# Optimization experiments

Hardware: AMD Instinct MI355X
Metric: run time of the kernel (lower is better)

## Reference

```python
import jax, jax.numpy as jnp
import numpy as np

ORDER = 3  # cubic B-splines, matching BSpline(..., 3)


def bspline_basis(x, t, order):
    """Cox-de Boor recursion, vectorized over batch and features.

    x: [B, F] evaluation points
    t: [F, M] sorted knot vectors (M = num_basis + order + 1)
    returns: [B, F, M-1-order] basis values B_j^{order}(x), zero outside the
    base interval [t[order], t[M-1-order]] (scipy extrapolate=False + nan_to_num).
    """
    M = t.shape[-1]
    xd = x[:, :, None]            # [B, F, 1]
    tb = t[None, :, :]            # [1, F, M]
    # degree-0 indicator functions: [B, F, M-1]
    B = ((xd >= tb[:, :, :-1]) & (xd < tb[:, :, 1:])).astype(x.dtype)
    for d in range(1, order + 1):
        t0 = tb[:, :, : M - d - 1]   # t_j
        td = tb[:, :, d : M - 1]     # t_{j+d}
        t1 = tb[:, :, 1 : M - d]     # t_{j+1}
        td1 = tb[:, :, d + 1 : M]    # t_{j+d+1}
        den1 = td - t0
        den2 = td1 - t1
        w1 = jnp.where(den1 > 0, (xd - t0) / jnp.where(den1 > 0, den1, 1.0), 0.0)
        w2 = jnp.where(den2 > 0, (td1 - xd) / jnp.where(den2 > 0, den2, 1.0), 0.0)
        B = w1 * B[:, :, : M - d - 1] + w2 * B[:, :, 1 : M - d]
    # zero outside the base interval [t[order], t[n]] (scipy NaN -> nan_to_num -> 0)
    lo = t[None, :, order]           # [1, F]
    hi = t[None, :, M - 1 - order]   # [1, F]
    valid = ((x >= lo) & (x <= hi)).astype(x.dtype)  # [B, F]
    return B * valid[:, :, None]


def setup_inputs() -> dict:
    key = jax.random.key(0)
    k_x, k_w, k_b = jax.random.split(key, 3)
    batch, in_features, out_features, num_basis = 4096, 512, 512, 30
    x = jax.random.normal(k_x, (batch, in_features), dtype=jnp.float32)
    knots = jnp.broadcast_to(
        jnp.linspace(-2.0, 2.0, num_basis + ORDER + 1, dtype=jnp.float32),
        (in_features, num_basis + ORDER + 1),
    )
    weights = jax.random.normal(k_w, (out_features, in_features, num_basis), dtype=jnp.float32)
    bias = jax.random.normal(k_b, (out_features,), dtype=jnp.float32)
    return {"x": x, "knots": knots, "weights": weights, "bias": bias}


def reference(x, knots, weights, bias):
    ks = jnp.sort(knots, axis=-1)              # module sorts knots before eval
    basis = bspline_basis(x, ks, ORDER)        # [B, F, num_basis]
    out = jnp.einsum("bij,kij->bk", basis, weights)
    return out + bias
```

## Files before the change

### kernel.cpp

```cpp
#include <hip/hip_runtime.h>
#include <hip/hip_bf16.h>
#include <stdint.h>


#define BATCH 4096
#define INF   512
#define OUTF  512
#define NB    30
#define NBP   32
#define NKNOT 34
#define KDIMP (INF * NBP)

#define BM 128
#define BN 128
#define BK 64
#define KSPLIT 8
#define KCHUNK (KDIMP / KSPLIT)
#define NT     (KCHUNK / BK)
#define FPC    (KCHUNK / NBP)

typedef short v8s __attribute__((ext_vector_type(8)));
typedef float v4f __attribute__((ext_vector_type(4)));

__device__ __forceinline__ unsigned short f2bf(float f) {
  uint32_t u = __float_as_uint(f);
  uint32_t r = (u + 0x7fffu + ((u >> 16) & 1u)) >> 16;
  return (unsigned short)r;
}

__device__ __forceinline__ void gload16(const unsigned short* g, unsigned short* l) {
  auto gp = reinterpret_cast<const __attribute__((address_space(1))) unsigned short*>(
      reinterpret_cast<uintptr_t>(g));
  auto lp = reinterpret_cast<__attribute__((address_space(3))) unsigned short*>(
      reinterpret_cast<uintptr_t>(l));
  __builtin_amdgcn_global_load_lds(gp, lp, 16, 0, 0);
}

__global__ __launch_bounds__(256) void w_cast_kernel(const float* __restrict__ in,
                                                     unsigned short* __restrict__ out) {
  int idx = blockIdx.x * 256 + threadIdx.x;
  int k   = idx >> 13;
  int rem = idx & 8191;
  int i   = rem >> 4;
  int jp  = rem & 15;
  int j   = jp * 2;
  const float* src = in + ((size_t)k * INF + i) * NB;
  float lo = (j     < NB) ? src[j]     : 0.f;
  float hi = (j + 1 < NB) ? src[j + 1] : 0.f;
  ((uint32_t*)out)[idx] = (uint32_t)f2bf(lo) | ((uint32_t)f2bf(hi) << 16);
}

__global__ __launch_bounds__(256) void basis_kernel(const float* __restrict__ x,
                                                    const float* __restrict__ knots,
                                                    uint2* __restrict__ valsT,
                                                    unsigned char* __restrict__ j0T) {
  __shared__ float tile[32][33];
  int b0 = blockIdx.x * 32;
  int f0 = blockIdx.y * 32;
  int lx = threadIdx.x & 31;
  int ly = threadIdx.x >> 5;
  #pragma unroll
  for (int q = 0; q < 4; ++q)
    tile[ly + q * 8][lx] = x[(size_t)(b0 + ly + q * 8) * INF + f0 + lx];
  __syncthreads();
  #pragma unroll
  for (int q = 0; q < 4; ++q) {
    int fy = ly + q * 8;
    float xv = tile[lx][fy];
    const float* tk = knots + (size_t)(f0 + fy) * NKNOT;
    uint2 pv = {0u, 0u};
    int j0 = 0;
    float tlo = tk[3], thi = tk[30];
    if (xv >= tlo && xv <= thi) {
      float t0v = tk[0];
      float h   = tk[1] - t0v;
      int m = (int)floorf((xv - t0v) * __builtin_amdgcn_rcpf(h));
      m = m < 3 ? 3 : (m > 30 ? 30 : m);
      while (m > 3 && xv < tk[m]) --m;
      while (m < 30 && xv >= tk[m + 1]) ++m;
      float Nv[4], left[4], right[4];
      Nv[0] = 1.f;
      #pragma unroll
      for (int d = 1; d <= 3; ++d) {
        left[d]  = xv - tk[m + 1 - d];
        right[d] = tk[m + d] - xv;
        float saved = 0.f;
        #pragma unroll
        for (int r = 0; r < d; ++r) {
          float temp = Nv[r] * __builtin_amdgcn_rcpf(right[r + 1] + left[d - r]);
          Nv[r] = saved + right[r + 1] * temp;
          saved = left[d - r] * temp;
        }
        Nv[d] = saved;
      }
      j0 = m - 3;
      pv.x = (uint32_t)f2bf(Nv[0]) | ((uint32_t)f2bf(Nv[1]) << 16);
      pv.y = (uint32_t)f2bf(Nv[2]) | ((uint32_t)f2bf(Nv[3]) << 16);
    }
    size_t oi = (size_t)(f0 + fy) * BATCH + b0 + lx;
    valsT[oi] = pv;
    j0T[oi]   = (unsigned char)j0;
  }
}

__global__ __launch_bounds__(256) void bias_kernel(const float* __restrict__ bias,
                                                   float* __restrict__ out) {
  int idx = blockIdx.x * 256 + threadIdx.x;
  out[idx] = bias[idx & (OUTF - 1)];
}

__device__ __forceinline__ void writeA(unsigned short* Abuf, int eb, int hf,
                                       uint2 v, int j0) {
  unsigned rowb = (unsigned)eb * 128;
  unsigned x7   = (unsigned)(eb & 7);
  char* base = (char*)Abuf;
  uint4 z = {0u, 0u, 0u, 0u};
  #pragma unroll
  for (int s = 0; s < 4; ++s) {
    unsigned slot = ((unsigned)(hf * 4 + s)) ^ x7;
    *(uint4*)(base + rowb + (slot << 4)) = z;
  }
  int d0 = hf * 16 + (j0 >> 1);
  #define WR32(d, val) { unsigned by = (unsigned)(d) * 4u; \
    *(uint32_t*)(base + rowb + ((((by >> 4) ^ x7) << 4) | (by & 15u))) = (val); }
  if (j0 & 1) {
    WR32(d0,     v.x << 16);
    WR32(d0 + 1, (v.x >> 16) | (v.y << 16));
    WR32(d0 + 2, v.y >> 16);
  } else {
    WR32(d0,     v.x);
    WR32(d0 + 1, v.y);
  }
  #undef WR32
}

__global__ __launch_bounds__(256, 4) void gemm_kernel(const uint2* __restrict__ valsT,
                                                      const unsigned char* __restrict__ j0T,
                                                      const unsigned short* __restrict__ Bt,
                                                      float* __restrict__ C) {
  __shared__ unsigned short As[BM * BK];
  __shared__ unsigned short Bs[BN * BK];
  int tid  = threadIdx.x;
  int lane = tid & 63;
  int w    = tid >> 6;

  int bid = blockIdx.x;
  int swz = (bid & 7) * 128 + (bid >> 3);
  int bn  = swz >> 8;
  int rem = swz & 255;
  int ks  = rem >> 5;
  int bm  = rem & 31;

  int row0 = bm * BM;
  int col0 = bn * BN;
  int kk0  = ks * KCHUNK;
  int fbase = ks * FPC;

  int eb = tid & 127;
  int hf = tid >> 7;
  size_t vidx0 = (size_t)(fbase + hf) * BATCH + row0 + eb;

  int lrow = lane >> 3;
  int lseg = (lane & 7) ^ lrow;
  const unsigned short* gb = Bt + (size_t)(col0 + w * 8 + lrow) * KDIMP + kk0 + lseg * 8;
  unsigned short* lB = &Bs[w * 512];

  v4f acc[4][4];
  #pragma unroll
  for (int i = 0; i < 4; ++i)
    #pragma unroll
    for (int j = 0; j < 4; ++j)
      acc[i][j] = (v4f){0.f, 0.f, 0.f, 0.f};

  int wr  = (w >> 1) & 1;
  int wc  = w & 1;
  int r16 = lane & 15;
  int kg  = lane >> 4;
  unsigned s0   = ((unsigned)kg ^ (unsigned)(r16 & 7)) << 4;
  unsigned aoff = (unsigned)(wr * 64 + r16) * 128;
  unsigned boff = (unsigned)(wc * 64 + r16) * 128;

  uint2 vc = valsT[vidx0];
  int   jc = j0T[vidx0];
  writeA(As, eb, hf, vc, jc);
  #pragma unroll
  for (int q = 0; q < 4; ++q)
    gload16(gb + (size_t)q * (32 * KDIMP), lB + q * 2048);
  uint2 vn = valsT[vidx0 + 8192];
  int   jn = j0T[vidx0 + 8192];
  __syncthreads();

  for (int t = 0; t < NT; ++t) {
    uint2 v2 = {0u, 0u};
    int   j2 = 0;
    if (t + 2 < NT) {
      size_t ix = vidx0 + (size_t)(t + 2) * 8192;
      v2 = valsT[ix];
      j2 = j0T[ix];
    }
    const char* Ab = (const char*)As;
    const char* Bb = (const char*)Bs;
    #pragma unroll
    for (int kc = 0; kc < 2; ++kc) {
      unsigned sk = s0 ^ (unsigned)(kc << 6);
      v8s af[4], bf[4];
      #pragma unroll
      for (int mi = 0; mi < 4; ++mi)
        af[mi] = *(const v8s*)(Ab + aoff + mi * 2048 + sk);
      #pragma unroll
      for (int ni = 0; ni < 4; ++ni)
        bf[ni] = *(const v8s*)(Bb + boff + ni * 2048 + sk);
      #pragma unroll
      for (int mi = 0; mi < 4; ++mi)
        #pragma unroll
        for (int ni = 0; ni < 4; ++ni)
          acc[mi][ni] = __builtin_amdgcn_mfma_f32_16x16x32_bf16(af[mi], bf[ni], acc[mi][ni], 0, 0, 0);
    }
    __syncthreads();
    if (t + 1 < NT) {
      writeA(As, eb, hf, vn, jn);
      const unsigned short* src = gb + (size_t)(t + 1) * BK;
      #pragma unroll
      for (int q = 0; q < 4; ++q)
        gload16(src + (size_t)q * (32 * KDIMP), lB + q * 2048);
      vn = v2; jn = j2;
      __syncthreads();
    }
  }

  int crow = (lane >> 4) * 4;
  int ccol = lane & 15;
  #pragma unroll
  for (int mi = 0; mi < 4; ++mi) {
    #pragma unroll
    for (int ni = 0; ni < 4; ++ni) {
      int r = row0 + wr * 64 + mi * 16 + crow;
      int c = col0 + wc * 64 + ni * 16 + ccol;
      #pragma unroll
      for (int q = 0; q < 4; ++q)
        atomicAdd(&C[(size_t)(r + q) * OUTF + c], acc[mi][ni][q]);
    }
  }
}

extern "C" void kernel_launch(void* const* d_in, const int* in_sizes, int n_in,
                              void* d_out, int out_size, void* d_ws, size_t ws_size,
                              hipStream_t stream) {
  const float* x     = (const float*)d_in[0];
  const float* knots = (const float*)d_in[1];
  const float* W     = (const float*)d_in[2];
  const float* bias  = (const float*)d_in[3];
  float* out = (float*)d_out;

  unsigned short* Wt    = (unsigned short*)d_ws;
  uint2*          valsT = (uint2*)((char*)d_ws + (size_t)OUTF * KDIMP * 2);
  unsigned char*  j0T   = (unsigned char*)((char*)d_ws + (size_t)OUTF * KDIMP * 2
                                           + (size_t)INF * BATCH * 8);

  w_cast_kernel<<<(OUTF * KDIMP / 2) / 256, 256, 0, stream>>>(W, Wt);
  basis_kernel<<<dim3(BATCH / 32, INF / 32), 256, 0, stream>>>(x, knots, valsT, j0T);
  bias_kernel<<<(BATCH * OUTF) / 256, 256, 0, stream>>>(bias, out);
  gemm_kernel<<<(BATCH / BM) * (OUTF / BN) * KSPLIT, 256, 0, stream>>>(valsT, j0T, Wt, out);
}
```

Measured before the change: 197.5 us.

## Build A fragments in registers from packed basis values, double-buffer B tile

```diff
diff --git a/kernel.cpp b/kernel.cpp
--- a/kernel.cpp
+++ b/kernel.cpp
@@ -34,6 +34,20 @@
   auto lp = reinterpret_cast<__attribute__((address_space(3))) unsigned short*>(
       reinterpret_cast<uintptr_t>(l));
   __builtin_amdgcn_global_load_lds(gp, lp, 16, 0, 0);
+}
+
+__device__ __forceinline__ v8s place4(uint64_t v, int d) {
+  int s = d * 16;
+  uint32_t ud = (uint32_t)d;
+  uint64_t vls    = v << (s & 63);
+  uint64_t vrs_hi = v >> ((64 - s) & 63);
+  uint64_t vrs_lo = v >> ((-s) & 63);
+  uint64_t lo = (ud <= 3u) ? vls : (((uint32_t)(-d) - 1u) <= 2u ? vrs_lo : 0ull);
+  uint64_t hi = ((ud - 1u) <= 2u) ? vrs_hi : (((ud - 4u) <= 3u) ? vls : 0ull);
+  union { uint32_t u[4]; v8s s8; } r;
+  r.u[0] = (uint32_t)lo; r.u[1] = (uint32_t)(lo >> 32);
+  r.u[2] = (uint32_t)hi; r.u[3] = (uint32_t)(hi >> 32);
+  return r.s8;
 }
 
 __global__ __launch_bounds__(256) void w_cast_kernel(const float* __restrict__ in,
@@ -52,8 +66,7 @@
 
 __global__ __launch_bounds__(256) void basis_kernel(const float* __restrict__ x,
                                                     const float* __restrict__ knots,
-                                                    uint2* __restrict__ valsT,
-                                                    unsigned char* __restrict__ j0T) {
+                                                    uint4* __restrict__ valsJ) {
   __shared__ float tile[32][33];
   int b0 = blockIdx.x * 32;
   int f0 = blockIdx.y * 32;
@@ -68,8 +81,7 @@
     int fy = ly + q * 8;
     float xv = tile[lx][fy];
     const float* tk = knots + (size_t)(f0 + fy) * NKNOT;
-    uint2 pv = {0u, 0u};
-    int j0 = 0;
+    uint4 pv = {0u, 0u, 0u, 0u};
     float tlo = tk[3], thi = tk[30];
     if (xv >= tlo && xv <= thi) {
       float t0v = tk[0];
@@ -93,13 +105,11 @@
         }
         Nv[d] = saved;
       }
-      j0 = m - 3;
       pv.x = (uint32_t)f2bf(Nv[0]) | ((uint32_t)f2bf(Nv[1]) << 16);
       pv.y = (uint32_t)f2bf(Nv[2]) | ((uint32_t)f2bf(Nv[3]) << 16);
-    }
-    size_t oi = (size_t)(f0 + fy) * BATCH + b0 + lx;
-    valsT[oi] = pv;
-    j0T[oi]   = (unsigned char)j0;
+      pv.z = (uint32_t)(m - 3);
+    }
+    valsJ[(size_t)(f0 + fy) * BATCH + b0 + lx] = pv;
   }
 }
 
@@ -109,37 +119,10 @@
   out[idx] = bias[idx & (OUTF - 1)];
 }
 
-__device__ __forceinline__ void writeA(unsigned short* Abuf, int eb, int hf,
-                                       uint2 v, int j0) {
-  unsigned rowb = (unsigned)eb * 128;
-  unsigned x7   = (unsigned)(eb & 7);
-  char* base = (char*)Abuf;
-  uint4 z = {0u, 0u, 0u, 0u};
-  #pragma unroll
-  for (int s = 0; s < 4; ++s) {
-    unsigned slot = ((unsigned)(hf * 4 + s)) ^ x7;
-    *(uint4*)(base + rowb + (slot << 4)) = z;
-  }
-  int d0 = hf * 16 + (j0 >> 1);
-  #define WR32(d, val) { unsigned by = (unsigned)(d) * 4u; \
-    *(uint32_t*)(base + rowb + ((((by >> 4) ^ x7) << 4) | (by & 15u))) = (val); }
-  if (j0 & 1) {
-    WR32(d0,     v.x << 16);
-    WR32(d0 + 1, (v.x >> 16) | (v.y << 16));
-    WR32(d0 + 2, v.y >> 16);
-  } else {
-    WR32(d0,     v.x);
-    WR32(d0 + 1, v.y);
-  }
-  #undef WR32
-}
-
-__global__ __launch_bounds__(256, 4) void gemm_kernel(const uint2* __restrict__ valsT,
-                                                      const unsigned char* __restrict__ j0T,
+__global__ __launch_bounds__(256, 3) void gemm_kernel(const uint4* __restrict__ valsJ,
                                                       const unsigned short* __restrict__ Bt,
                                                       float* __restrict__ C) {
-  __shared__ unsigned short As[BM * BK];
-  __shared__ unsigned short Bs[BN * BK];
+  __shared__ unsigned short Bs[2][BN * BK];
   int tid  = threadIdx.x;
   int lane = tid & 63;
   int w    = tid >> 6;
@@ -156,57 +139,66 @@
   int kk0  = ks * KCHUNK;
   int fbase = ks * FPC;
 
-  int eb = tid & 127;
-  int hf = tid >> 7;
-  size_t vidx0 = (size_t)(fbase + hf) * BATCH + row0 + eb;
-
-  int lrow = lane >> 3;
-  int lseg = (lane & 7) ^ lrow;
-  const unsigned short* gb = Bt + (size_t)(col0 + w * 8 + lrow) * KDIMP + kk0 + lseg * 8;
-  unsigned short* lB = &Bs[w * 512];
-
-  v4f acc[4][4];
-  #pragma unroll
-  for (int i = 0; i < 4; ++i)
-    #pragma unroll
-    for (int j = 0; j < 4; ++j)
-      acc[i][j] = (v4f){0.f, 0.f, 0.f, 0.f};
-
   int wr  = (w >> 1) & 1;
   int wc  = w & 1;
   int r16 = lane & 15;
   int kg  = lane >> 4;
+
+  int lrow = lane >> 3;
+  int lseg = (lane & 7) ^ lrow;
+  const unsigned short* gb = Bt + (size_t)(col0 + w * 8 + lrow) * KDIMP + kk0 + lseg * 8;
+
   unsigned s0   = ((unsigned)kg ^ (unsigned)(r16 & 7)) << 4;
-  unsigned aoff = (unsigned)(wr * 64 + r16) * 128;
   unsigned boff = (unsigned)(wc * 64 + r16) * 128;
 
-  uint2 vc = valsT[vidx0];
-  int   jc = j0T[vidx0];
-  writeA(As, eb, hf, vc, jc);
+  const uint4* vbase = valsJ + (size_t)fbase * BATCH + row0 + wr * 64 + r16;
+
+  v4f acc[4][4];
+  #pragma unroll
+  for (int i = 0; i < 4; ++i)
+    #pragma unroll
+    for (int j = 0; j < 4; ++j)
+      acc[i][j] = (v4f){0.f, 0.f, 0.f, 0.f};
+
+  uint4 pf[8];
+  #pragma unroll
+  for (int mi = 0; mi < 4; ++mi)
+    #pragma unroll
+    for (int hfi = 0; hfi < 2; ++hfi)
+      pf[mi * 2 + hfi] = vbase[(size_t)hfi * BATCH + mi * 16];
   #pragma unroll
   for (int q = 0; q < 4; ++q)
-    gload16(gb + (size_t)q * (32 * KDIMP), lB + q * 2048);
-  uint2 vn = valsT[vidx0 + 8192];
-  int   jn = j0T[vidx0 + 8192];
+    gload16(gb + (size_t)q * (32 * KDIMP), &Bs[0][w * 512 + q * 2048]);
   __syncthreads();
 
   for (int t = 0; t < NT; ++t) {
-    uint2 v2 = {0u, 0u};
-    int   j2 = 0;
-    if (t + 2 < NT) {
-      size_t ix = vidx0 + (size_t)(t + 2) * 8192;
-      v2 = valsT[ix];
-      j2 = j0T[ix];
-    }
-    const char* Ab = (const char*)As;
-    const char* Bb = (const char*)Bs;
+    int c = t & 1;
+    v8s af[2][4];
+    #pragma unroll
+    for (int mi = 0; mi < 4; ++mi)
+      #pragma unroll
+      for (int kc = 0; kc < 2; ++kc) {
+        uint4 p = pf[mi * 2 + kc];
+        uint64_t v = (uint64_t)p.x | ((uint64_t)p.y << 32);
+        af[kc][mi] = place4(v, (int)p.z - kg * 8);
+      }
+    if (t + 1 < NT) {
+      const unsigned short* src = gb + (size_t)(t + 1) * BK;
+      #pragma unroll
+      for (int q = 0; q < 4; ++q)
+        gload16(src + (size_t)q * (32 * KDIMP), &Bs[c ^ 1][w * 512 + q * 2048]);
+      size_t fo = (size_t)(2 * (t + 1)) * BATCH;
+      #pragma unroll
+      for (int mi = 0; mi < 4; ++mi)
+        #pragma unroll
+        for (int hfi = 0; hfi < 2; ++hfi)
+          pf[mi * 2 + hfi] = vbase[fo + (size_t)hfi * BATCH + mi * 16];
+    }
+    const char* Bb = (const char*)Bs[c];
     #pragma unroll
     for (int kc = 0; kc < 2; ++kc) {
       unsigned sk = s0 ^ (unsigned)(kc << 6);
-      v8s af[4], bf[4];
-      #pragma unroll
-      for (int mi = 0; mi < 4; ++mi)
-        af[mi] = *(const v8s*)(Ab + aoff + mi * 2048 + sk);
+      v8s bf[4];
       #pragma unroll
       for (int ni = 0; ni < 4; ++ni)
         bf[ni] = *(const v8s*)(Bb + boff + ni * 2048 + sk);
@@ -214,18 +206,9 @@
       for (int mi = 0; mi < 4; ++mi)
         #pragma unroll
         for (int ni = 0; ni < 4; ++ni)
-          acc[mi][ni] = __builtin_amdgcn_mfma_f32_16x16x32_bf16(af[mi], bf[ni], acc[mi][ni], 0, 0, 0);
+          acc[mi][ni] = __builtin_amdgcn_mfma_f32_16x16x32_bf16(af[kc][mi], bf[ni], acc[mi][ni], 0, 0, 0);
     }
     __syncthreads();
-    if (t + 1 < NT) {
-      writeA(As, eb, hf, vn, jn);
-      const unsigned short* src = gb + (size_t)(t + 1) * BK;
-      #pragma unroll
-      for (int q = 0; q < 4; ++q)
-        gload16(src + (size_t)q * (32 * KDIMP), lB + q * 2048);
-      vn = v2; jn = j2;
-      __syncthreads();
-    }
   }
 
   int crow = (lane >> 4) * 4;
@@ -253,12 +236,10 @@
   float* out = (float*)d_out;
 
   unsigned short* Wt    = (unsigned short*)d_ws;
-  uint2*          valsT = (uint2*)((char*)d_ws + (size_t)OUTF * KDIMP * 2);
-  unsigned char*  j0T   = (unsigned char*)((char*)d_ws + (size_t)OUTF * KDIMP * 2
-                                           + (size_t)INF * BATCH * 8);
+  uint4*          valsJ = (uint4*)((char*)d_ws + (size_t)OUTF * KDIMP * 2);
 
   w_cast_kernel<<<(OUTF * KDIMP / 2) / 256, 256, 0, stream>>>(W, Wt);
-  basis_kernel<<<dim3(BATCH / 32, INF / 32), 256, 0, stream>>>(x, knots, valsT, j0T);
+  basis_kernel<<<dim3(BATCH / 32, INF / 32), 256, 0, stream>>>(x, knots, valsJ);
   bias_kernel<<<(BATCH * OUTF) / 256, 256, 0, stream>>>(bias, out);
-  gemm_kernel<<<(BATCH / BM) * (OUTF / BN) * KSPLIT, 256, 0, stream>>>(valsT, j0T, Wt, out);
-}
+  gemm_kernel<<<(BATCH / BM) * (OUTF / BN) * KSPLIT, 256, 0, stream>>>(valsJ, Wt, out);
+}
```

New measurement: 215.8 us. 9.3% more time.
